# Kernel tuning notes

Measured on AMD Instinct MI355X. Metric: run time of the kernel, lower is better.

Reference implementation:

```python
import jax, jax.numpy as jnp
import numpy as np

DIM = 1024
HEADS = 16
MLP = 4096

def setup_inputs() -> dict:
    key = jax.random.key(0)
    ks = jax.random.split(key, 8)
    s = 0.02
    return {
        "x": jax.random.normal(ks[0], (4, 2048, DIM), dtype=jnp.float32),
        "W_qkv": jax.random.normal(ks[1], (DIM, 3 * DIM), dtype=jnp.float32) * s,
        "W_o": jax.random.normal(ks[2], (DIM, DIM), dtype=jnp.float32) * s,
        "b_o": jnp.zeros((DIM,), dtype=jnp.float32),
        "g1": jnp.ones((DIM,), dtype=jnp.float32),
        "be1": jnp.zeros((DIM,), dtype=jnp.float32),
        "W1": jax.random.normal(ks[3], (DIM, MLP), dtype=jnp.float32) * s,
        "b1": jnp.zeros((MLP,), dtype=jnp.float32),
        "W2": jax.random.normal(ks[4], (MLP, DIM), dtype=jnp.float32) * s,
        "b2": jnp.zeros((DIM,), dtype=jnp.float32),
        "g2": jnp.ones((DIM,), dtype=jnp.float32),
        "be2": jnp.zeros((DIM,), dtype=jnp.float32),
    }

def _gelu(x):
    # GELU approx used in source: x * sigmoid(1.702 * x)
    return x * jax.nn.sigmoid(1.702 * x)

def _layernorm(x, g, b, eps=1e-5):
    mu = jnp.mean(x, axis=-1, keepdims=True)
    var = jnp.var(x, axis=-1, keepdims=True)
    return (x - mu) * jax.lax.rsqrt(var + eps) * g + b

def reference(x, W_qkv, W_o, b_o, g1, be1, W1, b1, W2, b2, g2, be2):
    b, n, d = x.shape
    h = HEADS
    hd = d // h
    scale = hd ** -0.5
    qkv = x @ W_qkv                               # [b,n,3d]
    q, k, v = jnp.split(qkv, 3, axis=-1)
    q = q.reshape(b, n, h, hd).transpose(0, 2, 1, 3)  # [b,h,n,hd]
    k = k.reshape(b, n, h, hd).transpose(0, 2, 1, 3)
    v = v.reshape(b, n, h, hd).transpose(0, 2, 1, 3)
    dots = jnp.einsum('bhid,bhjd->bhij', q, k) * scale  # [b,h,n,n]
    attn = jax.nn.softmax(dots, axis=-1)
    out = jnp.einsum('bhij,bhjd->bhid', attn, v)
    out = out.transpose(0, 2, 1, 3).reshape(b, n, d)
    out = out @ W_o + b_o
    x = _layernorm(x + out, g1, be1)
    ff = _gelu(x @ W1 + b1) @ W2 + b2
    x = _layernorm(x + ff, g2, be2)
    return x
```

## Files before the change

### kernel.cpp

```cpp
#include <hip/hip_runtime.h>

typedef unsigned short u16;
typedef unsigned int u32;
typedef __attribute__((ext_vector_type(4))) float f32x4;
typedef __attribute__((ext_vector_type(16))) float f32x16;
typedef __attribute__((ext_vector_type(8))) __bf16 bf16x8;
typedef __attribute__((ext_vector_type(8))) unsigned short u16x8;
typedef __attribute__((ext_vector_type(4))) unsigned short u16x4;

__device__ __forceinline__ u16 f2bf(float f) {
  __bf16 h = (__bf16)f;
  union { __bf16 h; u16 u; } v; v.h = h;
  return v.u;
}

__device__ __forceinline__ float bf2f(u16 u) {
  union { unsigned u; float f; } v; v.u = ((unsigned)u) << 16;
  return v.f;
}

__device__ __forceinline__ u32 pk2(float a, float b) {
  return (u32)f2bf(a) | ((u32)f2bf(b) << 16);
}

__device__ __forceinline__ void async16(const void* g, void* l) {
  __builtin_amdgcn_global_load_lds(
      (const __attribute__((address_space(1))) unsigned int*)g,
      (__attribute__((address_space(3))) unsigned int*)l, 16, 0, 0);
}

__device__ __forceinline__ void barrier_f() {
  asm volatile("" ::: "memory");
  __builtin_amdgcn_s_barrier();
  asm volatile("" ::: "memory");
}

__global__ __launch_bounds__(256) void cvt_f32_bf16(const float* __restrict__ in,
                                                    u16* __restrict__ out, int n4) {
  int i = blockIdx.x * 256 + threadIdx.x;
  if (i >= n4) return;
  f32x4 v = *(const f32x4*)(in + (long)i * 4);
  u16x4 o;
#pragma unroll
  for (int j = 0; j < 4; j++) o[j] = f2bf(v[j]);
  *(u16x4*)(out + (long)i * 4) = o;
}

__global__ __launch_bounds__(256) void transpose_cvt(const float* __restrict__ W,
                                                     u16* __restrict__ Wt, int K, int N) {
  __shared__ float tile[32][33];
  int n0 = blockIdx.x * 32, k0 = blockIdx.y * 32;
  int tx = threadIdx.x & 31, ty = threadIdx.x >> 5;
#pragma unroll
  for (int i = 0; i < 32; i += 8)
    tile[ty + i][tx] = W[(long)(k0 + ty + i) * N + n0 + tx];
  __syncthreads();
#pragma unroll
  for (int i = 0; i < 32; i += 8)
    Wt[(long)(n0 + ty + i) * K + k0 + tx] = f2bf(tile[tx][ty + i]);
}

template <int BIAS, int GELU, int OBF, int QKV, int SPLITK>
__global__ __launch_bounds__(512, 1) void gemm8p(const u16* __restrict__ A,
                                                 const u16* __restrict__ Bt,
                                                 void* __restrict__ Cp,
                                                 const float* __restrict__ bias,
                                                 u16* __restrict__ kt2,
                                                 u16* __restrict__ vt2,
                                                 int M, int N, int Kst, int Klen) {
  __shared__ u16 As[2][256 * 64];
  __shared__ u16 Bs[2][256 * 64];
  const int t = threadIdx.x, wid = t >> 6, ln = t & 63;
  const int lr = ln & 15, lg = ln >> 4;
  const int wr = wid >> 2, wc = wid & 3;

  const int gx = gridDim.x, gy = gridDim.y;
  const int nwg = gx * gy * gridDim.z;
  const int flat = (blockIdx.z * gy + blockIdx.y) * gx + blockIdx.x;
  const int cpx = nwg >> 3;
  const int swz = (flat & 7) * cpx + (flat >> 3);
  const int sx = swz % gx, rest = swz / gx;
  const int sy = rest % gy, sz = rest / gy;
  const int m0 = sy * 256, n0 = sx * 256;
  const long zo = (long)sz * Klen;
  const int NT = Klen >> 6;

  const int srow = t >> 3;
  const int sch = ((t & 7) ^ (srow & 7)) * 8;
  const u16* gA = A + (long)(m0 + srow) * Kst + zo + sch;
  const u16* gB = Bt + (long)(n0 + srow) * Kst + zo + sch;
  const long KL = Kst;

#define STAGE_A(tt, h)                                                     \
  {                                                                        \
    const u16* s_ = gA + (long)((h) * 128) * KL + (long)(tt) * 64;         \
    char* d_ = (char*)As + ((tt) & 1) * 32768 + (h) * 16384 + wid * 1024;  \
    async16(s_, d_);                                                       \
    async16(s_ + 64 * KL, d_ + 8192);                                      \
  }
#define STAGE_B(tt, h)                                                     \
  {                                                                        \
    const u16* s_ = gB + (long)((h) * 128) * KL + (long)(tt) * 64;         \
    char* d_ = (char*)Bs + ((tt) & 1) * 32768 + (h) * 16384 + wid * 1024;  \
    async16(s_, d_);                                                       \
    async16(s_ + 64 * KL, d_ + 8192);                                      \
  }

  f32x4 acc[8][4] = {};
  const int cx0 = (lg ^ (lr & 7)) * 16;
  const int cx1 = ((4 + lg) ^ (lr & 7)) * 16;

  STAGE_A(0, 0); STAGE_A(0, 1);
  STAGE_B(0, 0); STAGE_B(0, 1);
  STAGE_A(1, 0); STAGE_A(1, 1);

  for (int tK = 0; tK < NT; ++tK) {
    const int cur = tK & 1;
    const char* ldsA = (const char*)As + cur * 32768;
    const char* ldsB = (const char*)Bs + cur * 32768;
    if (tK == NT - 1) {
      asm volatile("s_waitcnt vmcnt(0)" ::: "memory");
    } else {
      asm volatile("s_waitcnt vmcnt(4)" ::: "memory");
    }
    barrier_f();

    bf16x8 aLo[4][2], aHi[4][2], bLo[2][2], bHi[2][2];
#pragma unroll
    for (int mf = 0; mf < 4; mf++) {
      int row = wr * 128 + mf * 16 + lr;
      aLo[mf][0] = *(const bf16x8*)(ldsA + row * 128 + cx0);
      aLo[mf][1] = *(const bf16x8*)(ldsA + row * 128 + cx1);
    }
#pragma unroll
    for (int nf = 0; nf < 2; nf++) {
      int row = wc * 64 + nf * 16 + lr;
      bLo[nf][0] = *(const bf16x8*)(ldsB + row * 128 + cx0);
      bLo[nf][1] = *(const bf16x8*)(ldsB + row * 128 + cx1);
    }
    if (tK + 1 < NT) STAGE_B(tK + 1, 0);
    barrier_f();
    __builtin_amdgcn_s_setprio(1);
#pragma unroll
    for (int mf = 0; mf < 4; mf++)
#pragma unroll
      for (int nf = 0; nf < 2; nf++) {
        acc[mf][nf] = __builtin_amdgcn_mfma_f32_16x16x32_bf16(aLo[mf][0], bLo[nf][0], acc[mf][nf], 0, 0, 0);
        acc[mf][nf] = __builtin_amdgcn_mfma_f32_16x16x32_bf16(aLo[mf][1], bLo[nf][1], acc[mf][nf], 0, 0, 0);
      }
    __builtin_amdgcn_s_setprio(0);
    barrier_f();

#pragma unroll
    for (int mf = 0; mf < 4; mf++) {
      int row = wr * 128 + (mf + 4) * 16 + lr;
      aHi[mf][0] = *(const bf16x8*)(ldsA + row * 128 + cx0);
      aHi[mf][1] = *(const bf16x8*)(ldsA + row * 128 + cx1);
    }
    if (tK + 1 < NT) STAGE_B(tK + 1, 1);
    barrier_f();
    __builtin_amdgcn_s_setprio(1);
#pragma unroll
    for (int mf = 0; mf < 4; mf++)
#pragma unroll
      for (int nf = 0; nf < 2; nf++) {
        acc[mf + 4][nf] = __builtin_amdgcn_mfma_f32_16x16x32_bf16(aHi[mf][0], bLo[nf][0], acc[mf + 4][nf], 0, 0, 0);
        acc[mf + 4][nf] = __builtin_amdgcn_mfma_f32_16x16x32_bf16(aHi[mf][1], bLo[nf][1], acc[mf + 4][nf], 0, 0, 0);
      }
    __builtin_amdgcn_s_setprio(0);
    barrier_f();

#pragma unroll
    for (int nf = 0; nf < 2; nf++) {
      int row = wc * 64 + (nf + 2) * 16 + lr;
      bHi[nf][0] = *(const bf16x8*)(ldsB + row * 128 + cx0);
      bHi[nf][1] = *(const bf16x8*)(ldsB + row * 128 + cx1);
    }
    if (tK + 2 < NT) STAGE_A(tK + 2, 0);
    barrier_f();
    __builtin_amdgcn_s_setprio(1);
#pragma unroll
    for (int mf = 0; mf < 4; mf++)
#pragma unroll
      for (int nf = 0; nf < 2; nf++) {
        acc[mf][nf + 2] = __builtin_amdgcn_mfma_f32_16x16x32_bf16(aLo[mf][0], bHi[nf][0], acc[mf][nf + 2], 0, 0, 0);
        acc[mf][nf + 2] = __builtin_amdgcn_mfma_f32_16x16x32_bf16(aLo[mf][1], bHi[nf][1], acc[mf][nf + 2], 0, 0, 0);
      }
    __builtin_amdgcn_s_setprio(0);
    barrier_f();

    if (tK + 2 < NT) STAGE_A(tK + 2, 1);
    barrier_f();
    __builtin_amdgcn_s_setprio(1);
#pragma unroll
    for (int mf = 0; mf < 4; mf++)
#pragma unroll
      for (int nf = 0; nf < 2; nf++) {
        acc[mf + 4][nf + 2] = __builtin_amdgcn_mfma_f32_16x16x32_bf16(aHi[mf][0], bHi[nf][0], acc[mf + 4][nf + 2], 0, 0, 0);
        acc[mf + 4][nf + 2] = __builtin_amdgcn_mfma_f32_16x16x32_bf16(aHi[mf][1], bHi[nf][1], acc[mf + 4][nf + 2], 0, 0, 0);
      }
    __builtin_amdgcn_s_setprio(0);
    barrier_f();
  }
#undef STAGE_A
#undef STAGE_B

  u16* const Cu = (u16*)Cp + (SPLITK ? (long)sz * M * N : 0);
#pragma unroll
  for (int mf = 0; mf < 8; mf++) {
    int rbase = m0 + wr * 128 + mf * 16 + lg * 4;
#pragma unroll
    for (int nf = 0; nf < 4; nf++) {
      int col = n0 + wc * 64 + nf * 16 + lr;
      float bv = BIAS ? bias[col] : 0.f;
      if (QKV) {
        int bq = rbase >> 11;
        if (col < 1024) {
#pragma unroll
          for (int r = 0; r < 4; r++)
            ((u16*)Cp)[(long)(rbase + r) * 1024 + col] = f2bf(acc[mf][nf][r] * 0.18033688011112043f);
        } else if (col < 2048) {
          int hd = col - 1024, h_ = hd >> 6, d = hd & 63;
#pragma unroll
          for (int r = 0; r < 4; r++) {
            int key = (rbase + r) & 2047;
            kt2[((((long)(bq * 16 + h_) * 32 + (key >> 6)) * 8 + (d >> 3)) * 64 + (key & 63)) * 8 + (d & 7)] =
                f2bf(acc[mf][nf][r]);
          }
        } else {
          int hd = col - 2048, h_ = hd >> 6, d = hd & 63;
          int key0 = rbase & 2047;
          u16x4 o4;
#pragma unroll
          for (int r = 0; r < 4; r++) o4[r] = f2bf(acc[mf][nf][r]);
          *(u16x4*)&vt2[((((long)(bq * 16 + h_) * 32 + (key0 >> 6)) * 8 + ((key0 >> 3) & 7)) * 64 + d) * 8 + (key0 & 7)] = o4;
        }
      } else if (SPLITK) {
#pragma unroll
        for (int r = 0; r < 4; r++)
          Cu[(long)(rbase + r) * N + col] = f2bf(acc[mf][nf][r]);
      } else {
#pragma unroll
        for (int r = 0; r < 4; r++) {
          float v = acc[mf][nf][r] + bv;
          if (GELU) v = v / (1.f + __expf(-1.702f * v));
          if (OBF) ((u16*)Cp)[(long)(rbase + r) * N + col] = f2bf(v);
          else ((float*)Cp)[(long)(rbase + r) * N + col] = v;
        }
      }
    }
  }
}

__global__ __launch_bounds__(512, 4) void attn_kernel(const u16* __restrict__ qb,
                                                      const u16* __restrict__ kt2,
                                                      const u16* __restrict__ vt2,
                                                      u16* __restrict__ out) {
  const int bh = blockIdx.y, h = bh & 15;
  const int q0 = blockIdx.x * 256;
  const int t = threadIdx.x, wv = t >> 6, ln = t & 63;
  const int lq = ln & 31, hi = ln >> 5;
  __shared__ u16 Ks[2][4096];
  __shared__ u16 Vs[2][4096];
  const long tok0 = (long)(bh >> 4) * 2048;

  bf16x8 bQ[4];
  {
    long row = tok0 + q0 + wv * 32 + lq;
    const u16* qp = &qb[row * 1024 + h * 64 + hi * 8];
#pragma unroll
    for (int c = 0; c < 4; c++) bQ[c] = *(const bf16x8*)(qp + c * 16);
  }

  const int isK = (t < 256);
  const int tt = t & 255;
  const u16* gS = (isK ? kt2 : vt2) + (long)bh * 131072 + tt * 8;
  char* const dS = (isK ? (char*)&Ks[0][0] : (char*)&Vs[0][0]) + (wv & 3) * 1024;

  f32x16 accO0 = {}, accO1 = {};
  float accLs = 0.f;

  async16(gS, dS);
  async16(gS + 2048, dS + 4096);
  gS += 4096;

  for (int it = 0; it < 32; ++it) {
    const int cur = it & 1;
    if (it < 31) {
      char* nS = dS + (cur ^ 1) * 8192;
      async16(gS, nS);
      async16(gS + 2048, nS + 4096);
      gS += 4096;
      asm volatile("s_waitcnt vmcnt(2)" ::: "memory");
    } else {
      asm volatile("s_waitcnt vmcnt(0)" ::: "memory");
    }
    __builtin_amdgcn_s_barrier();
    __builtin_amdgcn_sched_barrier(0);
    const u16* Kc = &Ks[cur][0];
    const u16* Vc = &Vs[cur][0];

    u32 frag[4][4];
#pragma unroll
    for (int kb = 0; kb < 2; kb++) {
      f32x16 s = {};
      __builtin_amdgcn_s_setprio(1);
#pragma unroll
      for (int c = 0; c < 4; c++) {
        bf16x8 aK = *(const bf16x8*)&Kc[((c * 2 + hi) * 64 + kb * 32 + lq) * 8];
        s = __builtin_amdgcn_mfma_f32_32x32x16_bf16(aK, bQ[c], s, 0, 0, 0);
      }
      __builtin_amdgcn_s_setprio(0);
      float pv[16];
#pragma unroll
      for (int r = 0; r < 16; r++) { pv[r] = exp2f(s[r]); accLs += pv[r]; }
#pragma unroll
      for (int cc = 0; cc < 2; cc++) {
        u32 dA0 = pk2(pv[8 * cc + 0], pv[8 * cc + 1]);
        u32 dA1 = pk2(pv[8 * cc + 2], pv[8 * cc + 3]);
        u32 dB0 = pk2(pv[8 * cc + 4], pv[8 * cc + 5]);
        u32 dB1 = pk2(pv[8 * cc + 6], pv[8 * cc + 7]);
        u32 e0 = (u32)__shfl_xor((int)dA0, 32);
        u32 e1 = (u32)__shfl_xor((int)dA1, 32);
        u32 f0 = (u32)__shfl_xor((int)dB0, 32);
        u32 f1 = (u32)__shfl_xor((int)dB1, 32);
        frag[kb * 2 + cc][0] = hi ? f0 : dA0;
        frag[kb * 2 + cc][1] = hi ? f1 : dA1;
        frag[kb * 2 + cc][2] = hi ? dB0 : e0;
        frag[kb * 2 + cc][3] = hi ? dB1 : e1;
      }
    }

    __builtin_amdgcn_s_setprio(1);
#pragma unroll
    for (int c2 = 0; c2 < 4; c2++) {
      union { u32 u[4]; bf16x8 v; } pb;
      pb.u[0] = frag[c2][0]; pb.u[1] = frag[c2][1];
      pb.u[2] = frag[c2][2]; pb.u[3] = frag[c2][3];
      bf16x8 aV0 = *(const bf16x8*)&Vc[((c2 * 2 + hi) * 64 + lq) * 8];
      bf16x8 aV1 = *(const bf16x8*)&Vc[((c2 * 2 + hi) * 64 + 32 + lq) * 8];
      accO0 = __builtin_amdgcn_mfma_f32_32x32x16_bf16(aV0, pb.v, accO0, 0, 0, 0);
      accO1 = __builtin_amdgcn_mfma_f32_32x32x16_bf16(aV1, pb.v, accO1, 0, 0, 0);
    }
    __builtin_amdgcn_s_setprio(0);
    __builtin_amdgcn_s_barrier();
    __builtin_amdgcn_sched_barrier(0);
  }

  float lT = accLs + __shfl_xor(accLs, 32);
  float inv = 1.f / lT;
  long tq = tok0 + q0 + wv * 32 + lq;
  u16* op = &out[tq * 1024 + h * 64 + hi * 4];
#pragma unroll
  for (int qd = 0; qd < 4; qd++) {
    u16x4 o4, o5;
#pragma unroll
    for (int j = 0; j < 4; j++) {
      o4[j] = f2bf(accO0[qd * 4 + j] * inv);
      o5[j] = f2bf(accO1[qd * 4 + j] * inv);
    }
    *(u16x4*)(op + qd * 8) = o4;
    *(u16x4*)(op + 32 + qd * 8) = o5;
  }
}

template <int XBF, int OF32>
__global__ __launch_bounds__(256) void ln_kernel(const void* __restrict__ xin,
                                                 const u16* __restrict__ p0,
                                                 const u16* __restrict__ p1,
                                                 const float* __restrict__ bias,
                                                 const float* __restrict__ g,
                                                 const float* __restrict__ be,
                                                 float* __restrict__ of,
                                                 u16* __restrict__ ob) {
  int row = blockIdx.x, t = threadIdx.x;
  long base = (long)row * 1024 + t * 4;
  f32x4 a;
  if (XBF) {
    u16x4 xa = *((const u16x4*)xin + row * 256 + t);
#pragma unroll
    for (int j = 0; j < 4; j++) a[j] = bf2f(xa[j]);
  } else {
    a = *((const f32x4*)xin + row * 256 + t);
  }
  u16x4 u0 = *(const u16x4*)(p0 + base);
  u16x4 u1 = *(const u16x4*)(p1 + base);
  f32x4 bb4 = *(const f32x4*)(bias + t * 4);
  f32x4 v;
#pragma unroll
  for (int j = 0; j < 4; j++) v[j] = a[j] + bf2f(u0[j]) + bf2f(u1[j]) + bb4[j];
  float s = v[0] + v[1] + v[2] + v[3];
  float ss = v[0] * v[0] + v[1] * v[1] + v[2] * v[2] + v[3] * v[3];
#pragma unroll
  for (int o = 1; o < 64; o <<= 1) { s += __shfl_xor(s, o); ss += __shfl_xor(ss, o); }
  __shared__ float sm[8];
  if ((t & 63) == 0) { sm[t >> 6] = s; sm[4 + (t >> 6)] = ss; }
  __syncthreads();
  s = sm[0] + sm[1] + sm[2] + sm[3];
  ss = sm[4] + sm[5] + sm[6] + sm[7];
  float mu = s * 0.0009765625f;
  float var = ss * 0.0009765625f - mu * mu;
  float inv = rsqrtf(var + 1e-5f);
  f32x4 gg = *(const f32x4*)(g + t * 4);
  f32x4 bb = *(const f32x4*)(be + t * 4);
  f32x4 y;
#pragma unroll
  for (int j = 0; j < 4; j++) y[j] = (v[j] - mu) * inv * gg[j] + bb[j];
  if (OF32) {
    *(f32x4*)(of + base) = y;
  } else {
    u16x4 o4;
#pragma unroll
    for (int j = 0; j < 4; j++) o4[j] = f2bf(y[j]);
    *(u16x4*)(ob + base) = o4;
  }
}

extern "C" void kernel_launch(void* const* d_in, const int* in_sizes, int n_in,
                              void* d_out, int out_size, void* d_ws, size_t ws_size,
                              hipStream_t stream) {
  const float* x = (const float*)d_in[0];
  const float* Wqkv = (const float*)d_in[1];
  const float* Wo = (const float*)d_in[2];
  const float* bo = (const float*)d_in[3];
  const float* g1 = (const float*)d_in[4];
  const float* be1 = (const float*)d_in[5];
  const float* W1 = (const float*)d_in[6];
  const float* b1 = (const float*)d_in[7];
  const float* W2 = (const float*)d_in[8];
  const float* b2 = (const float*)d_in[9];
  const float* g2 = (const float*)d_in[10];
  const float* be2 = (const float*)d_in[11];
  float* out = (float*)d_out;
  char* ws = (char*)d_ws;

  u16* xb = (u16*)(ws + 0);
  u16* qb = (u16*)(ws + 16777216);
  u16* kt2b = (u16*)(ws + 33554432);
  u16* vt2b = (u16*)(ws + 50331648);
  u16* h1b = (u16*)(ws + 0);
  u16* attnb = (u16*)(ws + 67108864);
  u16* x1b = (u16*)(ws + 83886080);
  u16* pp = (u16*)(ws + 100663296);
  u16* ffp = (u16*)(ws + 100663296);
  u16* wqkvt = (u16*)(ws + 134217728);
  u16* wot = (u16*)(ws + 140509184);
  u16* w1t = (u16*)(ws + 142606336);
  u16* w2t = (u16*)(ws + 150994944);

  cvt_f32_bf16<<<8192, 256, 0, stream>>>(x, xb, 2097152);
  transpose_cvt<<<dim3(96, 32), 256, 0, stream>>>(Wqkv, wqkvt, 1024, 3072);
  transpose_cvt<<<dim3(32, 32), 256, 0, stream>>>(Wo, wot, 1024, 1024);
  transpose_cvt<<<dim3(128, 32), 256, 0, stream>>>(W1, w1t, 1024, 4096);
  transpose_cvt<<<dim3(32, 128), 256, 0, stream>>>(W2, w2t, 4096, 1024);
  gemm8p<0, 0, 0, 1, 0><<<dim3(12, 32, 1), 512, 0, stream>>>(
      xb, wqkvt, qb, nullptr, kt2b, vt2b, 8192, 3072, 1024, 1024);
  attn_kernel<<<dim3(8, 64), 512, 0, stream>>>(qb, kt2b, vt2b, attnb);
  gemm8p<0, 0, 0, 0, 1><<<dim3(4, 32, 2), 512, 0, stream>>>(
      attnb, wot, pp, nullptr, nullptr, nullptr, 8192, 1024, 1024, 512);
  ln_kernel<0, 0><<<8192, 256, 0, stream>>>(x, pp, pp + (long)8192 * 1024, bo,
                                            g1, be1, nullptr, x1b);
  gemm8p<1, 1, 1, 0, 0><<<dim3(16, 32, 1), 512, 0, stream>>>(
      x1b, w1t, h1b, b1, nullptr, nullptr, 8192, 4096, 1024, 1024);
  gemm8p<0, 0, 0, 0, 1><<<dim3(4, 32, 2), 512, 0, stream>>>(
      h1b, w2t, ffp, nullptr, nullptr, nullptr, 8192, 1024, 4096, 2048);
  ln_kernel<1, 1><<<8192, 256, 0, stream>>>(x1b, ffp, ffp + (long)8192 * 1024, b2,
                                            g2, be2, out, nullptr);
}
```

Before: 398.6 us.

## Double attention KV tile per barrier and compute row sums via MFMA with ones

The attention kernel now loads 128 keys per pipeline stage instead of 64, processing two sub-tiles per barrier pair, which halves the loop iterations and barriers. The softmax denominator is now accumulated with an extra MFMA against a ones vector using the bf16-rounded probabilities, replacing the per-element scalar adds and the final shuffle. This doubles LDS use per block (64KB) and may reduce occupancy, and it adds MFMA work to the PV stage.

```diff
diff --git a/kernel.cpp b/kernel.cpp
--- a/kernel.cpp
+++ b/kernel.cpp
@@ -260,8 +260,8 @@
   const int q0 = blockIdx.x * 256;
   const int t = threadIdx.x, wv = t >> 6, ln = t & 63;
   const int lq = ln & 31, hi = ln >> 5;
-  __shared__ u16 Ks[2][4096];
-  __shared__ u16 Vs[2][4096];
+  __shared__ u16 Ks[2][8192];
+  __shared__ u16 Vs[2][8192];
   const long tok0 = (long)(bh >> 4) * 2048;
 
   bf16x8 bQ[4];
@@ -277,78 +277,89 @@
   const u16* gS = (isK ? kt2 : vt2) + (long)bh * 131072 + tt * 8;
   char* const dS = (isK ? (char*)&Ks[0][0] : (char*)&Vs[0][0]) + (wv & 3) * 1024;
 
-  f32x16 accO0 = {}, accO1 = {};
-  float accLs = 0.f;
-
-  async16(gS, dS);
-  async16(gS + 2048, dS + 4096);
-  gS += 4096;
-
-  for (int it = 0; it < 32; ++it) {
+  f32x16 accO0 = {}, accO1 = {}, accL = {};
+
+  bf16x8 aOnes;
+  {
+    union { u16x8 u; bf16x8 b; } ou;
+#pragma unroll
+    for (int j = 0; j < 8; j++) ou.u[j] = 0x3F80;
+    aOnes = ou.b;
+  }
+
+#pragma unroll
+  for (int i = 0; i < 4; i++) async16(gS + i * 2048, dS + i * 4096);
+  gS += 8192;
+
+  for (int it = 0; it < 16; ++it) {
     const int cur = it & 1;
-    if (it < 31) {
-      char* nS = dS + (cur ^ 1) * 8192;
-      async16(gS, nS);
-      async16(gS + 2048, nS + 4096);
-      gS += 4096;
-      asm volatile("s_waitcnt vmcnt(2)" ::: "memory");
+    if (it < 15) {
+      char* nS = dS + (cur ^ 1) * 16384;
+#pragma unroll
+      for (int i = 0; i < 4; i++) async16(gS + i * 2048, nS + i * 4096);
+      gS += 8192;
+      asm volatile("s_waitcnt vmcnt(4)" ::: "memory");
     } else {
       asm volatile("s_waitcnt vmcnt(0)" ::: "memory");
     }
     __builtin_amdgcn_s_barrier();
     __builtin_amdgcn_sched_barrier(0);
-    const u16* Kc = &Ks[cur][0];
-    const u16* Vc = &Vs[cur][0];
-
-    u32 frag[4][4];
-#pragma unroll
-    for (int kb = 0; kb < 2; kb++) {
-      f32x16 s = {};
+
+#pragma unroll
+    for (int sub = 0; sub < 2; ++sub) {
+      const u16* Kc = &Ks[cur][sub * 4096];
+      const u16* Vc = &Vs[cur][sub * 4096];
+
+      u32 frag[4][4];
+#pragma unroll
+      for (int kb = 0; kb < 2; kb++) {
+        f32x16 s = {};
+        __builtin_amdgcn_s_setprio(1);
+#pragma unroll
+        for (int c = 0; c < 4; c++) {
+          bf16x8 aK = *(const bf16x8*)&Kc[((c * 2 + hi) * 64 + kb * 32 + lq) * 8];
+          s = __builtin_amdgcn_mfma_f32_32x32x16_bf16(aK, bQ[c], s, 0, 0, 0);
+        }
+        __builtin_amdgcn_s_setprio(0);
+        float pv[16];
+#pragma unroll
+        for (int r = 0; r < 16; r++) pv[r] = exp2f(s[r]);
+#pragma unroll
+        for (int cc = 0; cc < 2; cc++) {
+          u32 dA0 = pk2(pv[8 * cc + 0], pv[8 * cc + 1]);
+          u32 dA1 = pk2(pv[8 * cc + 2], pv[8 * cc + 3]);
+          u32 dB0 = pk2(pv[8 * cc + 4], pv[8 * cc + 5]);
+          u32 dB1 = pk2(pv[8 * cc + 6], pv[8 * cc + 7]);
+          u32 e0 = (u32)__shfl_xor((int)dA0, 32);
+          u32 e1 = (u32)__shfl_xor((int)dA1, 32);
+          u32 f0 = (u32)__shfl_xor((int)dB0, 32);
+          u32 f1 = (u32)__shfl_xor((int)dB1, 32);
+          frag[kb * 2 + cc][0] = hi ? f0 : dA0;
+          frag[kb * 2 + cc][1] = hi ? f1 : dA1;
+          frag[kb * 2 + cc][2] = hi ? dB0 : e0;
+          frag[kb * 2 + cc][3] = hi ? dB1 : e1;
+        }
+      }
+
       __builtin_amdgcn_s_setprio(1);
 #pragma unroll
-      for (int c = 0; c < 4; c++) {
-        bf16x8 aK = *(const bf16x8*)&Kc[((c * 2 + hi) * 64 + kb * 32 + lq) * 8];
-        s = __builtin_amdgcn_mfma_f32_32x32x16_bf16(aK, bQ[c], s, 0, 0, 0);
+      for (int c2 = 0; c2 < 4; c2++) {
+        union { u32 u[4]; bf16x8 v; } pb;
+        pb.u[0] = frag[c2][0]; pb.u[1] = frag[c2][1];
+        pb.u[2] = frag[c2][2]; pb.u[3] = frag[c2][3];
+        bf16x8 aV0 = *(const bf16x8*)&Vc[((c2 * 2 + hi) * 64 + lq) * 8];
+        bf16x8 aV1 = *(const bf16x8*)&Vc[((c2 * 2 + hi) * 64 + 32 + lq) * 8];
+        accL = __builtin_amdgcn_mfma_f32_32x32x16_bf16(aOnes, pb.v, accL, 0, 0, 0);
+        accO0 = __builtin_amdgcn_mfma_f32_32x32x16_bf16(aV0, pb.v, accO0, 0, 0, 0);
+        accO1 = __builtin_amdgcn_mfma_f32_32x32x16_bf16(aV1, pb.v, accO1, 0, 0, 0);
       }
       __builtin_amdgcn_s_setprio(0);
-      float pv[16];
-#pragma unroll
-      for (int r = 0; r < 16; r++) { pv[r] = exp2f(s[r]); accLs += pv[r]; }
-#pragma unroll
-      for (int cc = 0; cc < 2; cc++) {
-        u32 dA0 = pk2(pv[8 * cc + 0], pv[8 * cc + 1]);
-        u32 dA1 = pk2(pv[8 * cc + 2], pv[8 * cc + 3]);
-        u32 dB0 = pk2(pv[8 * cc + 4], pv[8 * cc + 5]);
-        u32 dB1 = pk2(pv[8 * cc + 6], pv[8 * cc + 7]);
-        u32 e0 = (u32)__shfl_xor((int)dA0, 32);
-        u32 e1 = (u32)__shfl_xor((int)dA1, 32);
-        u32 f0 = (u32)__shfl_xor((int)dB0, 32);
-        u32 f1 = (u32)__shfl_xor((int)dB1, 32);
-        frag[kb * 2 + cc][0] = hi ? f0 : dA0;
-        frag[kb * 2 + cc][1] = hi ? f1 : dA1;
-        frag[kb * 2 + cc][2] = hi ? dB0 : e0;
-        frag[kb * 2 + cc][3] = hi ? dB1 : e1;
-      }
-    }
-
-    __builtin_amdgcn_s_setprio(1);
-#pragma unroll
-    for (int c2 = 0; c2 < 4; c2++) {
-      union { u32 u[4]; bf16x8 v; } pb;
-      pb.u[0] = frag[c2][0]; pb.u[1] = frag[c2][1];
-      pb.u[2] = frag[c2][2]; pb.u[3] = frag[c2][3];
-      bf16x8 aV0 = *(const bf16x8*)&Vc[((c2 * 2 + hi) * 64 + lq) * 8];
-      bf16x8 aV1 = *(const bf16x8*)&Vc[((c2 * 2 + hi) * 64 + 32 + lq) * 8];
-      accO0 = __builtin_amdgcn_mfma_f32_32x32x16_bf16(aV0, pb.v, accO0, 0, 0, 0);
-      accO1 = __builtin_amdgcn_mfma_f32_32x32x16_bf16(aV1, pb.v, accO1, 0, 0, 0);
-    }
-    __builtin_amdgcn_s_setprio(0);
+    }
     __builtin_amdgcn_s_barrier();
     __builtin_amdgcn_sched_barrier(0);
   }
 
-  float lT = accLs + __shfl_xor(accLs, 32);
-  float inv = 1.f / lT;
+  float inv = 1.f / accL[0];
   long tq = tok0 + q0 + wv * 32 + lq;
   u16* op = &out[tq * 1024 + h * 64 + hi * 4];
 #pragma unroll
```

Result: no change. 398.9 us (+0.1%).
